# Performance work log

Measured on AMD Instinct MI355X. Metric: run time of the kernel, lower is better.

## Reference

```python
import jax, jax.numpy as jnp
import numpy as np

N_CHARS = 256
EMB = 1024
HID = 2048
SEQ = 8192

def setup_inputs() -> dict:
    key = jax.random.key(0)
    ks = jax.random.split(key, 7)
    s = 0.02
    return {
        "input_seq": jax.random.randint(ks[0], (SEQ,), 0, N_CHARS),
        "emb": jax.random.normal(ks[1], (N_CHARS, EMB), jnp.float32) * s,
        "wax_w": jax.random.normal(ks[2], (HID, EMB), jnp.float32) * s,
        "wax_b": jnp.zeros((HID,), jnp.float32),
        "waa_w": jax.random.normal(ks[3], (HID, HID), jnp.float32) * s,
        "wya_w": jax.random.normal(ks[4], (N_CHARS, HID), jnp.float32) * s,
        "wya_b": jnp.zeros((N_CHARS,), jnp.float32),
    }

def reference(input_seq, emb, wax_w, wax_b, waa_w, wya_w, wya_b):
    # Embed whole sequence: [T, E]
    x_seq = emb[input_seq]
    # Precompute the input projection for all steps (parallel GEMM): [T, H]
    xa_seq = x_seq @ wax_w.T + wax_b

    def step(h, xa):
        h_new = jnp.tanh(xa + h @ waa_w.T)  # [H]
        o = h_new @ wya_w.T + wya_b          # [n_chars]
        return h_new, o

    h0 = jnp.zeros((HID,), x_seq.dtype)
    h_final, out = jax.lax.scan(step, h0, xa_seq)
    # out: [T, n_chars]; hidden returned as [1, H] to match torch module
    return out, h_final[None, :]
```

## Files before the change

kernel.cpp:

```cpp
#include <hip/hip_runtime.h>
#include <stdint.h>

#define SEQ 8192
#define EMB 1024
#define HID 2048
#define NCH 256

#define SCAN_B 64
#define SCAN_T 512
#define ROWS_PB (HID / SCAN_B)
#define SENT 0xFFFFFFFFu
#define NREP 4
#define NSLOT 8

typedef unsigned uint4v __attribute__((ext_vector_type(4)));

__global__ __launch_bounds__(256) void gemm_tn(const float* __restrict__ X,
                                               const float* __restrict__ W,
                                               const float* __restrict__ bias,
                                               float* __restrict__ C,
                                               int M, int N, int K)
{
    __shared__ float Xs[16][68];
    __shared__ float Ws[16][68];
    const int m0 = blockIdx.x * 64, n0 = blockIdx.y * 64;
    const int tid  = threadIdx.x;
    const int lrow = tid >> 2;
    const int kq   = (tid & 3) * 4;
    const int tx   = tid & 15, ty = tid >> 4;
    float acc[4][4] = {};
    const float* Xp = X + (size_t)(m0 + lrow) * K + kq;
    const float* Wp = W + (size_t)(n0 + lrow) * K + kq;

    for (int k0 = 0; k0 < K; k0 += 16) {
        float4 xv = *(const float4*)(Xp + k0);
        float4 wv = *(const float4*)(Wp + k0);
        __syncthreads();
        Xs[kq+0][lrow] = xv.x; Xs[kq+1][lrow] = xv.y;
        Xs[kq+2][lrow] = xv.z; Xs[kq+3][lrow] = xv.w;
        Ws[kq+0][lrow] = wv.x; Ws[kq+1][lrow] = wv.y;
        Ws[kq+2][lrow] = wv.z; Ws[kq+3][lrow] = wv.w;
        __syncthreads();
#pragma unroll
        for (int kk = 0; kk < 16; ++kk) {
            float4 av = *(const float4*)&Xs[kk][ty * 4];
            float4 bv = *(const float4*)&Ws[kk][tx * 4];
            float a[4] = {av.x, av.y, av.z, av.w};
            float b[4] = {bv.x, bv.y, bv.z, bv.w};
#pragma unroll
            for (int i = 0; i < 4; ++i)
#pragma unroll
                for (int j = 0; j < 4; ++j)
                    acc[i][j] += a[i] * b[j];
        }
    }
#pragma unroll
    for (int i = 0; i < 4; ++i) {
        const int m = m0 + ty * 4 + i;
#pragma unroll
        for (int j = 0; j < 4; ++j) {
            const int n = n0 + tx * 4 + j;
            C[(size_t)m * N + n] = acc[i][j] + bias[n];
        }
    }
}

__device__ __forceinline__ float fast_tanh(float x)
{
    float e = __builtin_amdgcn_exp2f(x * 2.885390081777927f);
    return 1.0f - 2.0f * __builtin_amdgcn_rcpf(e + 1.0f);
}

__global__ __launch_bounds__(SCAN_T, 2) void rnn_scan(
    const int*  __restrict__ seq,
    const float* __restrict__ waa,
    const float* __restrict__ P,
    float* __restrict__ H,
    unsigned* __restrict__ ring)
{
    const int b    = blockIdx.x;
    const int tid  = threadIdx.x;
    const int wv   = tid >> 6;
    const int lane = tid & 63;
    const int R0   = b * ROWS_PB + wv * 4;
    const int rep  = b & (NREP - 1);

    __shared__ float hbuf[2][HID];

    float w0[32], w1[32], w2[32], w3[32];
#pragma unroll
    for (int j = 0; j < 8; ++j) {
        const float* base = waa + 256 * j + 4 * lane;
        float4 a = *(const float4*)(base + (size_t)(R0 + 0) * HID);
        float4 c = *(const float4*)(base + (size_t)(R0 + 1) * HID);
        float4 d = *(const float4*)(base + (size_t)(R0 + 2) * HID);
        float4 e = *(const float4*)(base + (size_t)(R0 + 3) * HID);
        w0[4*j+0]=a.x; w0[4*j+1]=a.y; w0[4*j+2]=a.z; w0[4*j+3]=a.w;
        w1[4*j+0]=c.x; w1[4*j+1]=c.y; w1[4*j+2]=c.z; w1[4*j+3]=c.w;
        w2[4*j+0]=d.x; w2[4*j+1]=d.y; w2[4*j+2]=d.z; w2[4*j+3]=d.w;
        w3[4*j+0]=e.x; w3[4*j+1]=e.y; w3[4*j+2]=e.z; w3[4*j+3]=e.w;
    }
#pragma unroll
    for (int k = 0; k < 32; ++k) {
        asm volatile("" : "+v"(w0[k])); asm volatile("" : "+v"(w1[k]));
        asm volatile("" : "+v"(w2[k])); asm volatile("" : "+v"(w3[k]));
    }

    unsigned* myring = ring + (size_t)rep * NSLOT * HID;

    for (int t = 0; t < SEQ; ++t) {
        const int ch = seq[t];
        float xav = 0.f;
        if (lane < 4) xav = P[(size_t)ch * HID + R0 + lane];

        {
            const unsigned long long* p8 = (const unsigned long long*)
                (myring + (size_t)(t & (NSLOT - 1)) * HID + tid * 4);
            unsigned long long a = __hip_atomic_load(p8 + 0, __ATOMIC_RELAXED,
                                                     __HIP_MEMORY_SCOPE_AGENT);
            unsigned long long c = __hip_atomic_load(p8 + 1, __ATOMIC_RELAXED,
                                                     __HIP_MEMORY_SCOPE_AGENT);
            while (((unsigned)a == SENT) || ((unsigned)(a >> 32) == SENT) ||
                   ((unsigned)c == SENT) || ((unsigned)(c >> 32) == SENT)) {
                __builtin_amdgcn_s_sleep(1);
                a = __hip_atomic_load(p8 + 0, __ATOMIC_RELAXED,
                                      __HIP_MEMORY_SCOPE_AGENT);
                c = __hip_atomic_load(p8 + 1, __ATOMIC_RELAXED,
                                      __HIP_MEMORY_SCOPE_AGENT);
            }
            uint4v v;
            v.x = (unsigned)a; v.y = (unsigned)(a >> 32);
            v.z = (unsigned)c; v.w = (unsigned)(c >> 32);
            *(uint4v*)&hbuf[t & 1][tid * 4] = v;
        }
        __syncthreads();

        float a0 = 0.f, a1 = 0.f, a2 = 0.f, a3 = 0.f;
        const float* hb = &hbuf[t & 1][4 * lane];
#pragma unroll
        for (int j = 0; j < 8; ++j) {
            float4 hv = *(const float4*)(hb + 256 * j);
            a0 += w0[4*j+0]*hv.x + w0[4*j+1]*hv.y + w0[4*j+2]*hv.z + w0[4*j+3]*hv.w;
            a1 += w1[4*j+0]*hv.x + w1[4*j+1]*hv.y + w1[4*j+2]*hv.z + w1[4*j+3]*hv.w;
            a2 += w2[4*j+0]*hv.x + w2[4*j+1]*hv.y + w2[4*j+2]*hv.z + w2[4*j+3]*hv.w;
            a3 += w3[4*j+0]*hv.x + w3[4*j+1]*hv.y + w3[4*j+2]*hv.z + w3[4*j+3]*hv.w;
        }
        a0 += __shfl_xor(a0, 1, 64);
        a1 += __shfl_xor(a1, 1, 64);
        a2 += __shfl_xor(a2, 1, 64);
        a3 += __shfl_xor(a3, 1, 64);
        float m01 = (lane & 1) ? a1 : a0;
        float m23 = (lane & 1) ? a3 : a2;
        m01 += __shfl_xor(m01, 2, 64);
        m23 += __shfl_xor(m23, 2, 64);
        float m = (lane & 2) ? m23 : m01;
        m += __shfl_xor(m, 4, 64);
        m += __shfl_xor(m, 8, 64);
        m += __shfl_xor(m, 16, 64);
        m += __shfl_xor(m, 32, 64);

        if (lane < 4) {
            float hn = fast_tanh(xav + m);
            const unsigned hu = __float_as_uint(hn);
            const int row = R0 + lane;
            const int s1 = (t + 1) & (NSLOT - 1);
            const int s5 = (t + 5) & (NSLOT - 1);
#pragma unroll
            for (int r = 0; r < NREP; ++r) {
                unsigned* rb = ring + (size_t)r * NSLOT * HID;
                __hip_atomic_store(rb + (size_t)s1 * HID + row, hu,
                                   __ATOMIC_RELAXED, __HIP_MEMORY_SCOPE_AGENT);
                __hip_atomic_store(rb + (size_t)s5 * HID + row, SENT,
                                   __ATOMIC_RELAXED, __HIP_MEMORY_SCOPE_AGENT);
            }
            H[(size_t)(t + 1) * HID + row] = hn;
        }
    }
}

__global__ void copy_h(const float* __restrict__ src, float* __restrict__ dst)
{
    int i = blockIdx.x * blockDim.x + threadIdx.x;
    if (i < HID) dst[i] = src[i];
}

extern "C" void kernel_launch(void* const* d_in, const int* in_sizes, int n_in,
                              void* d_out, int out_size, void* d_ws, size_t ws_size,
                              hipStream_t stream)
{
    const int*   seq  = (const int*)  d_in[0];
    const float* emb  = (const float*)d_in[1];
    const float* wax  = (const float*)d_in[2];
    const float* waxb = (const float*)d_in[3];
    const float* waa  = (const float*)d_in[4];
    const float* wya  = (const float*)d_in[5];
    const float* wyab = (const float*)d_in[6];
    float* out = (float*)d_out;

    float*    H    = (float*)d_ws;
    float*    P    = (float*)((char*)d_ws + (size_t)(SEQ + 1) * HID * sizeof(float));
    unsigned* ring = (unsigned*)(P + (size_t)NCH * HID);

    (void)hipMemsetAsync(ring, 0xFF, (size_t)NREP * NSLOT * HID * sizeof(unsigned), stream);
    for (int r = 0; r < NREP; ++r)
        (void)hipMemsetAsync(ring + (size_t)r * NSLOT * HID, 0,
                             HID * sizeof(unsigned), stream);

    dim3 gA(NCH / 64, HID / 64);
    gemm_tn<<<gA, 256, 0, stream>>>(emb, wax, waxb, P, NCH, HID, EMB);

    rnn_scan<<<SCAN_B, SCAN_T, 0, stream>>>(seq, waa, P, H, ring);

    dim3 gC(SEQ / 64, NCH / 64);
    gemm_tn<<<gC, 256, 0, stream>>>(H + HID, wya, wyab, out, SEQ, NCH, HID);

    copy_h<<<(HID + 255) / 256, 256, 0, stream>>>(H + (size_t)SEQ * HID,
                                                  out + (size_t)SEQ * NCH);
}
```

Before: 15.56 ms.

## Prefetch next hidden-state ring slot speculatively and halve scan block size

Switches the recurrent scan to 128 blocks of 256 threads, so each block owns 16 rows and each thread loads 8 hidden values per step. The hidden-state load for the next step is issued right after the reduction using inline-asm system-coherent loads, and the next iteration only re-polls if any sentinel is still present. The goal is to hide cross-block ring polling latency behind the tanh/store work. This relies on hand-written s_waitcnt counts, which is fragile if the compiler reorders other memory ops. Ring stores are also regrouped so all value stores go out before the sentinel stores.

Result: slower. 18.86 ms (+21.2%).

```diff
diff --git a/kernel.cpp b/kernel.cpp
--- a/kernel.cpp
+++ b/kernel.cpp
@@ -6,8 +6,8 @@
 #define HID 2048
 #define NCH 256
 
-#define SCAN_B 64
-#define SCAN_T 512
+#define SCAN_B 128
+#define SCAN_T 256
 #define ROWS_PB (HID / SCAN_B)
 #define SENT 0xFFFFFFFFu
 #define NREP 4
@@ -71,7 +71,7 @@
     return 1.0f - 2.0f * __builtin_amdgcn_rcpf(e + 1.0f);
 }
 
-__global__ __launch_bounds__(SCAN_T, 2) void rnn_scan(
+__global__ __launch_bounds__(SCAN_T, 1) void rnn_scan(
     const int*  __restrict__ seq,
     const float* __restrict__ waa,
     const float* __restrict__ P,
@@ -107,32 +107,31 @@
     }
 
     unsigned* myring = ring + (size_t)rep * NSLOT * HID;
-
+    const uint4v SV = {SENT, SENT, SENT, SENT};
+    uint4v v0 = SV, v1 = SV;
+
+#pragma unroll 1
     for (int t = 0; t < SEQ; ++t) {
         const int ch = seq[t];
         float xav = 0.f;
         if (lane < 4) xav = P[(size_t)ch * HID + R0 + lane];
 
-        {
-            const unsigned long long* p8 = (const unsigned long long*)
-                (myring + (size_t)(t & (NSLOT - 1)) * HID + tid * 4);
-            unsigned long long a = __hip_atomic_load(p8 + 0, __ATOMIC_RELAXED,
-                                                     __HIP_MEMORY_SCOPE_AGENT);
-            unsigned long long c = __hip_atomic_load(p8 + 1, __ATOMIC_RELAXED,
-                                                     __HIP_MEMORY_SCOPE_AGENT);
-            while (((unsigned)a == SENT) || ((unsigned)(a >> 32) == SENT) ||
-                   ((unsigned)c == SENT) || ((unsigned)(c >> 32) == SENT)) {
-                __builtin_amdgcn_s_sleep(1);
-                a = __hip_atomic_load(p8 + 0, __ATOMIC_RELAXED,
-                                      __HIP_MEMORY_SCOPE_AGENT);
-                c = __hip_atomic_load(p8 + 1, __ATOMIC_RELAXED,
-                                      __HIP_MEMORY_SCOPE_AGENT);
-            }
-            uint4v v;
-            v.x = (unsigned)a; v.y = (unsigned)(a >> 32);
-            v.z = (unsigned)c; v.w = (unsigned)(c >> 32);
-            *(uint4v*)&hbuf[t & 1][tid * 4] = v;
-        }
+        asm volatile("s_waitcnt vmcnt(9)" : "+v"(v0), "+v"(v1) : : "memory");
+        if (v0.x == SENT || v0.y == SENT || v0.z == SENT || v0.w == SENT ||
+            v1.x == SENT || v1.y == SENT || v1.z == SENT || v1.w == SENT) {
+            const unsigned* pp =
+                myring + (size_t)(t & (NSLOT - 1)) * HID + tid * 8;
+            do {
+                asm volatile("s_waitcnt vmcnt(0)\n\t"
+                             "global_load_dwordx4 %0, %2, off sc0 sc1\n\t"
+                             "global_load_dwordx4 %1, %2, off offset:16 sc0 sc1\n\t"
+                             "s_waitcnt vmcnt(0)"
+                             : "+v"(v0), "+v"(v1) : "v"(pp) : "memory");
+            } while (v0.x == SENT || v0.y == SENT || v0.z == SENT || v0.w == SENT ||
+                     v1.x == SENT || v1.y == SENT || v1.z == SENT || v1.w == SENT);
+        }
+        *(uint4v*)&hbuf[t & 1][tid * 8]     = v0;
+        *(uint4v*)&hbuf[t & 1][tid * 8 + 4] = v1;
         __syncthreads();
 
         float a0 = 0.f, a1 = 0.f, a2 = 0.f, a3 = 0.f;
@@ -159,6 +158,15 @@
         m += __shfl_xor(m, 16, 64);
         m += __shfl_xor(m, 32, 64);
 
+        if (t + 1 < SEQ) {
+            const unsigned* pn =
+                myring + (size_t)((t + 1) & (NSLOT - 1)) * HID + tid * 8;
+            v0 = SV; v1 = SV;
+            asm volatile("global_load_dwordx4 %0, %2, off sc0 sc1\n\t"
+                         "global_load_dwordx4 %1, %2, off offset:16 sc0 sc1"
+                         : "+v"(v0), "+v"(v1) : "v"(pn) : "memory");
+        }
+
         if (lane < 4) {
             float hn = fast_tanh(xav + m);
             const unsigned hu = __float_as_uint(hn);
@@ -166,13 +174,15 @@
             const int s1 = (t + 1) & (NSLOT - 1);
             const int s5 = (t + 5) & (NSLOT - 1);
 #pragma unroll
-            for (int r = 0; r < NREP; ++r) {
-                unsigned* rb = ring + (size_t)r * NSLOT * HID;
-                __hip_atomic_store(rb + (size_t)s1 * HID + row, hu,
-                                   __ATOMIC_RELAXED, __HIP_MEMORY_SCOPE_AGENT);
-                __hip_atomic_store(rb + (size_t)s5 * HID + row, SENT,
-                                   __ATOMIC_RELAXED, __HIP_MEMORY_SCOPE_AGENT);
-            }
+            for (int r = 0; r < NREP; ++r)
+                __hip_atomic_store(ring + ((size_t)r * NSLOT + s1) * HID + row,
+                                   hu, __ATOMIC_RELAXED,
+                                   __HIP_MEMORY_SCOPE_AGENT);
+#pragma unroll
+            for (int r = 0; r < NREP; ++r)
+                __hip_atomic_store(ring + ((size_t)r * NSLOT + s5) * HID + row,
+                                   SENT, __ATOMIC_RELAXED,
+                                   __HIP_MEMORY_SCOPE_AGENT);
             H[(size_t)(t + 1) * HID + row] = hn;
         }
     }
```
